# Kernel tuning notes

Hardware: AMD Instinct MI355X
Metric: run time of the kernel (lower is better)

Reference implementation:

```python
import jax, jax.numpy as jnp
import numpy as np

D_MODEL = 512
N_HEADS = 8
Q_SEQ_LEN = 1024
KV_SEQ_LEN = 1024
N_MODES = 64
D_HEAD = D_MODEL // N_HEADS

# FEDformer frequency_modes (deterministic/lowest branch): lowest n_modes freqs
Q_MODES = np.arange(min(N_MODES, Q_SEQ_LEN // 2))
KV_MODES = np.arange(min(N_MODES, KV_SEQ_LEN // 2))


def setup_inputs() -> dict:
    key = jax.random.key(0)
    kq, kk, kv, kwr, kwi = jax.random.split(key, 5)
    B = 8
    scale = 1.0 / (D_MODEL * D_MODEL)
    return {
        "query": jax.random.normal(kq, (B, N_HEADS, Q_SEQ_LEN, D_HEAD), jnp.float32),
        "key": jax.random.normal(kk, (B, N_HEADS, KV_SEQ_LEN, D_HEAD), jnp.float32),
        "value": jax.random.normal(kv, (B, N_HEADS, KV_SEQ_LEN, D_HEAD), jnp.float32),
        "weights_re": scale * jax.random.uniform(kwr, (N_HEADS, D_HEAD, D_HEAD, len(Q_MODES)), jnp.float32),
        "weights_im": scale * jax.random.uniform(kwi, (N_HEADS, D_HEAD, D_HEAD, len(Q_MODES)), jnp.float32),
    }


def reference(query, key, value, weights_re, weights_im):
    # value is accepted but unused by the original forward (FEA-f variant).
    B, H, L, D = query.shape
    q_modes = jnp.asarray(Q_MODES)
    kv_modes = jnp.asarray(KV_MODES)

    # [B,H,D,L] -> rfft along time -> gather selected frequency modes
    q_fft = jnp.fft.rfft(jnp.swapaxes(query, -2, -1), axis=-1)   # [B,H,D,L//2+1]
    k_fft = jnp.fft.rfft(jnp.swapaxes(key, -2, -1), axis=-1)     # [B,H,D,Lk//2+1]
    q_fft = jnp.take(q_fft, q_modes, axis=-1)                    # [B,H,D,Mq]
    k_fft = jnp.take(k_fft, kv_modes, axis=-1)                   # [B,H,D,Mk]

    # complex attention in frequency domain (no conjugation, as in torch einsum)
    scores_fft = jnp.einsum('bhdq,bhdk->bhqk', q_fft, k_fft)
    attn_fft = jnp.tanh(scores_fft)
    context_fft = jnp.einsum('bhqk,bhdk->bhdq', attn_fft, k_fft)  # [B,H,D,Mq]

    w = (weights_re + 1j * weights_im).astype(jnp.complex64)      # [H,D,D,Mq]
    context_fft = jnp.einsum('bhiq,hijq->bhjq', context_fft, w)   # [B,H,D,Mq]

    # scatter modes back into full rfft spectrum, then irfft
    out_fft = jnp.zeros((B, H, D, L // 2 + 1), jnp.complex64)
    out_fft = out_fft.at[..., q_modes].set(context_fft)
    d_model = H * D
    context = jnp.fft.irfft(out_fft / d_model / d_model, n=L, axis=-1)  # [B,H,D,L]
    return context
```

## Files before the change

### kernel.cpp

```cpp
#include <hip/hip_runtime.h>
#include <hip/hip_bf16.h>
#include <cmath>

#define BATCH 8
#define NH 8
#define BH 64
#define SEQ 1024
#define DH 64
#define NM 64

#define P_PLANE 4096
#define C2_OFF  4194304

__global__ __launch_bounds__(256) void k_dft(const float* __restrict__ q,
                                             const float* __restrict__ k,
                                             float* __restrict__ P) {
  const int bid = blockIdx.x;
  const int bh = bid & 63;
  const int inp = (bid >> 6) & 1;
  const int th = bid >> 7;
  const float* x = (inp ? k : q) + (size_t)bh * (SEQ * DH);

  __shared__ float xs[64][64];
  const int tid = threadIdx.x;
  const int dg = tid & 7;
  const int mg = tid >> 3;
  const int d0 = dg * 8;

  float accr[2][8] = {{0.f}}, acci[2][8] = {{0.f}};

  float stepc[2], steps_[2];
#pragma unroll
  for (int mi = 0; mi < 2; ++mi) {
    float ph = (float)(mg * 2 + mi) * (1.0f / 512.0f);
    stepc[mi] = cospif(ph);
    steps_[mi] = -sinpif(ph);
  }

  for (int ch = 0; ch < 8; ++ch) {
    const int t0g = th * 512 + ch * 64;
    const float4* src = reinterpret_cast<const float4*>(x + (size_t)t0g * DH);
    float4* dst = reinterpret_cast<float4*>(&xs[0][0]);
#pragma unroll
    for (int i = 0; i < 4; ++i) dst[tid + i * 256] = src[tid + i * 256];
    __syncthreads();

    float wr[2], wi[2];
#pragma unroll
    for (int mi = 0; mi < 2; ++mi) {
      int m = mg * 2 + mi;
      int p0 = (m * t0g) & 1023;
      float ph = (float)p0 * (1.0f / 512.0f);
      wr[mi] = cospif(ph);
      wi[mi] = -sinpif(ph);
    }

#pragma unroll 4
    for (int t = 0; t < 64; ++t) {
      float4 a = *reinterpret_cast<const float4*>(&xs[t][d0]);
      float4 b = *reinterpret_cast<const float4*>(&xs[t][d0 + 4]);
      float xv[8] = {a.x, a.y, a.z, a.w, b.x, b.y, b.z, b.w};
#pragma unroll
      for (int mi = 0; mi < 2; ++mi) {
        float cwr = wr[mi], cwi = wi[mi];
#pragma unroll
        for (int di = 0; di < 8; ++di) {
          accr[mi][di] = fmaf(cwr, xv[di], accr[mi][di]);
          acci[mi][di] = fmaf(cwi, xv[di], acci[mi][di]);
        }
        float nr = cwr * stepc[mi] - cwi * steps_[mi];
        float ni = cwr * steps_[mi] + cwi * stepc[mi];
        wr[mi] = nr; wi[mi] = ni;
      }
    }
    __syncthreads();
  }

  const size_t base = ((((size_t)inp * 2 + th) * 64 + bh) * 2) * P_PLANE;
#pragma unroll
  for (int mi = 0; mi < 2; ++mi) {
    int m = mg * 2 + mi;
    float* pr = P + base + (size_t)m * 64 + d0;
    float* pi = P + base + P_PLANE + (size_t)m * 64 + d0;
    *reinterpret_cast<float4*>(pr)     = make_float4(accr[mi][0], accr[mi][1], accr[mi][2], accr[mi][3]);
    *reinterpret_cast<float4*>(pr + 4) = make_float4(accr[mi][4], accr[mi][5], accr[mi][6], accr[mi][7]);
    *reinterpret_cast<float4*>(pi)     = make_float4(acci[mi][0], acci[mi][1], acci[mi][2], acci[mi][3]);
    *reinterpret_cast<float4*>(pi + 4) = make_float4(acci[mi][4], acci[mi][5], acci[mi][6], acci[mi][7]);
  }
}

__device__ __forceinline__ void ctanh_f(float x, float y, float& rr, float& ri) {
  float a = 2.0f * x, b = 2.0f * y;
  if (fabsf(a) > 20.0f) {
    rr = (a > 0.0f) ? 1.0f : -1.0f;
    ri = 0.0f;
  } else {
    float ea = expf(a), ena = expf(-a);
    float sb, cb;
    sincosf(b, &sb, &cb);
    float den = 0.5f * (ea + ena) + cb;
    rr = 0.5f * (ea - ena) / den;
    ri = sb / den;
  }
}

__global__ __launch_bounds__(256) void k_mid(const float* __restrict__ P,
                                             const float* __restrict__ wre,
                                             const float* __restrict__ wim,
                                             float* __restrict__ C2) {
  __shared__ float Kr[64][67], Ki[64][67];
  __shared__ float Qr[16][67], Qi[16][67];
  __shared__ float Ar[16][67], Ai[16][67];
  __shared__ float C1r[64][17], C1i[64][17];

  const int tid = threadIdx.x;
  const int bh = blockIdx.x >> 2;
  const int qq = blockIdx.x & 3;
  const int h = bh & 7;

  const size_t pq0 = (((size_t)0 * 2 + 0) * 64 + bh) * 2 * P_PLANE;
  const size_t pq1 = (((size_t)0 * 2 + 1) * 64 + bh) * 2 * P_PLANE;
  const size_t pk0 = (((size_t)1 * 2 + 0) * 64 + bh) * 2 * P_PLANE;
  const size_t pk1 = (((size_t)1 * 2 + 1) * 64 + bh) * 2 * P_PLANE;

  for (int idx = tid; idx < 4096; idx += 256) {
    int kk = idx >> 6, dd = idx & 63;
    Kr[kk][dd] = P[pk0 + idx] + P[pk1 + idx];
    Ki[kk][dd] = P[pk0 + P_PLANE + idx] + P[pk1 + P_PLANE + idx];
  }
  for (int idx = tid; idx < 1024; idx += 256) {
    int qi2 = idx >> 6, dd = idx & 63;
    int m = qq * 16 + qi2;
    Qr[qi2][dd] = P[pq0 + m * 64 + dd] + P[pq1 + m * 64 + dd];
    Qi[qi2][dd] = P[pq0 + P_PLANE + m * 64 + dd] + P[pq1 + P_PLANE + m * 64 + dd];
  }
  __syncthreads();

  {
    const int q = tid >> 4, k0 = (tid & 15) * 4;
    float sr[4] = {0.f}, si[4] = {0.f};
    for (int d = 0; d < 64; ++d) {
      float qr = Qr[q][d], qi = Qi[q][d];
#pragma unroll
      for (int j = 0; j < 4; ++j) {
        float kr = Kr[k0 + j][d], ki = Ki[k0 + j][d];
        sr[j] = fmaf(qr, kr, sr[j]); sr[j] = fmaf(-qi, ki, sr[j]);
        si[j] = fmaf(qr, ki, si[j]); si[j] = fmaf(qi, kr, si[j]);
      }
    }
#pragma unroll
    for (int j = 0; j < 4; ++j) {
      float rr, ri;
      ctanh_f(sr[j], si[j], rr, ri);
      Ar[q][k0 + j] = rr;
      Ai[q][k0 + j] = ri;
    }
  }
  __syncthreads();

  {
    const int q = tid >> 4, d0 = (tid & 15) * 4;
    float cr[4] = {0.f}, ci[4] = {0.f};
    for (int kk = 0; kk < 64; ++kk) {
      float ar = Ar[q][kk], ai = Ai[q][kk];
#pragma unroll
      for (int j = 0; j < 4; ++j) {
        float kr = Kr[kk][d0 + j], ki = Ki[kk][d0 + j];
        cr[j] = fmaf(ar, kr, cr[j]); cr[j] = fmaf(-ai, ki, cr[j]);
        ci[j] = fmaf(ar, ki, ci[j]); ci[j] = fmaf(ai, kr, ci[j]);
      }
    }
#pragma unroll
    for (int j = 0; j < 4; ++j) { C1r[d0 + j][q] = cr[j]; C1i[d0 + j][q] = ci[j]; }
  }
  __syncthreads();

  {
    const int ql = tid & 15, j0 = (tid >> 4) * 4;
    const int qg = qq * 16 + ql;
    float ar[4] = {0.f}, ai[4] = {0.f};
    for (int i = 0; i < 64; ++i) {
      float c1r = C1r[i][ql], c1i = C1i[i][ql];
      const size_t wb = (((size_t)h * 64 + i) * 64 + j0) * 64 + qg;
#pragma unroll
      for (int j = 0; j < 4; ++j) {
        float wr = wre[wb + (size_t)j * 64];
        float wi = wim[wb + (size_t)j * 64];
        ar[j] = fmaf(c1r, wr, ar[j]); ar[j] = fmaf(-c1i, wi, ar[j]);
        ai[j] = fmaf(c1r, wi, ai[j]); ai[j] = fmaf(c1i, wr, ai[j]);
      }
    }
#pragma unroll
    for (int j = 0; j < 4; ++j) {
      size_t o = (((size_t)bh * 64 + qg) * 64 + (j0 + j)) * 2;
      C2[o] = ar[j];
      C2[o + 1] = ai[j];
    }
  }
}

__global__ __launch_bounds__(256) void k_idft(const float* __restrict__ C2,
                                              float* __restrict__ out) {
  __shared__ float Cr[64][68], Ci[64][68];
  const int tid = threadIdx.x;
  const int bh = blockIdx.x >> 3;
  const int tc = blockIdx.x & 7;
  const float s = 1.0f / (512.0f * 512.0f * 1024.0f);

  for (int idx = tid; idx < 4096; idx += 256) {
    int m = idx >> 6, j = idx & 63;
    float f = (m == 0) ? s : 2.0f * s;
    Cr[m][j] = f * C2[((size_t)bh * 4096 + idx) * 2];
    Ci[m][j] = f * C2[((size_t)bh * 4096 + idx) * 2 + 1];
  }
  __syncthreads();

  const int tt = tid & 31, jg = tid >> 5;
  const int t0 = tc * 128 + tt * 4, j0 = jg * 8;

  float wc[4], wsn[4], sc[4], ss[4];
#pragma unroll
  for (int kk = 0; kk < 4; ++kk) {
    float ph = (float)((t0 + kk) & 1023) * (1.0f / 512.0f);
    sc[kk] = cospif(ph);
    ss[kk] = sinpif(ph);
    wc[kk] = 1.0f;
    wsn[kk] = 0.0f;
  }

  float acc[4][8] = {{0.f}};
  for (int m = 0; m < 64; ++m) {
    float4 c0 = *reinterpret_cast<const float4*>(&Cr[m][j0]);
    float4 c1 = *reinterpret_cast<const float4*>(&Cr[m][j0 + 4]);
    float4 e0 = *reinterpret_cast<const float4*>(&Ci[m][j0]);
    float4 e1 = *reinterpret_cast<const float4*>(&Ci[m][j0 + 4]);
    float crv[8] = {c0.x, c0.y, c0.z, c0.w, c1.x, c1.y, c1.z, c1.w};
    float civ[8] = {e0.x, e0.y, e0.z, e0.w, e1.x, e1.y, e1.z, e1.w};
#pragma unroll
    for (int kk = 0; kk < 4; ++kk) {
      float cw = wc[kk], sw = wsn[kk];
#pragma unroll
      for (int jj = 0; jj < 8; ++jj) {
        acc[kk][jj] = fmaf(crv[jj], cw, acc[kk][jj]);
        acc[kk][jj] = fmaf(-civ[jj], sw, acc[kk][jj]);
      }
      float nr = cw * sc[kk] - sw * ss[kk];
      float ni = cw * ss[kk] + sw * sc[kk];
      wc[kk] = nr; wsn[kk] = ni;
    }
  }

#pragma unroll
  for (int jj = 0; jj < 8; ++jj) {
    float4 v = make_float4(acc[0][jj], acc[1][jj], acc[2][jj], acc[3][jj]);
    *reinterpret_cast<float4*>(&out[(size_t)bh * 65536 + (size_t)(j0 + jj) * 1024 + t0]) = v;
  }
}

extern "C" void kernel_launch(void* const* d_in, const int* in_sizes, int n_in,
                              void* d_out, int out_size, void* d_ws, size_t ws_size,
                              hipStream_t stream) {
  const float* q   = (const float*)d_in[0];
  const float* k   = (const float*)d_in[1];
  const float* wre = (const float*)d_in[3];
  const float* wim = (const float*)d_in[4];
  float* out = (float*)d_out;
  float* ws  = (float*)d_ws;

  float* P  = ws;
  float* C2 = ws + C2_OFF;

  k_dft <<<256, 256, 0, stream>>>(q, k, P);
  k_mid <<<256, 256, 0, stream>>>(P, wre, wim, C2);
  k_idft<<<512, 256, 0, stream>>>(C2, out);
}
```

Baseline: 190.9 us.

## Split mode-mixing into separate kernel and double grid sizes for DFT and iDFT

After: 178.1 us. 1.07x faster.

```diff
diff --git a/kernel.cpp b/kernel.cpp
--- a/kernel.cpp
+++ b/kernel.cpp
@@ -10,7 +10,10 @@
 #define NM 64
 
 #define P_PLANE 4096
-#define C2_OFF  4194304
+#define P_FLOATS (2*4*64*2*4096)
+#define C1R_OFF  P_FLOATS
+#define C1I_OFF  (C1R_OFF + 64*64*64)
+#define C2_OFF   (C1I_OFF + 64*64*64)
 
 __global__ __launch_bounds__(256) void k_dft(const float* __restrict__ q,
                                              const float* __restrict__ k,
@@ -18,74 +21,62 @@
   const int bid = blockIdx.x;
   const int bh = bid & 63;
   const int inp = (bid >> 6) & 1;
-  const int th = bid >> 7;
+  const int tq = bid >> 7;
   const float* x = (inp ? k : q) + (size_t)bh * (SEQ * DH);
 
   __shared__ float xs[64][64];
   const int tid = threadIdx.x;
-  const int dg = tid & 7;
-  const int mg = tid >> 3;
-  const int d0 = dg * 8;
-
-  float accr[2][8] = {{0.f}}, acci[2][8] = {{0.f}};
-
-  float stepc[2], steps_[2];
-#pragma unroll
-  for (int mi = 0; mi < 2; ++mi) {
-    float ph = (float)(mg * 2 + mi) * (1.0f / 512.0f);
-    stepc[mi] = cospif(ph);
-    steps_[mi] = -sinpif(ph);
-  }
-
-  for (int ch = 0; ch < 8; ++ch) {
-    const int t0g = th * 512 + ch * 64;
+  const int m = tid >> 2;
+  const int d0 = (tid & 3) * 16;
+
+  float accr[16] = {0.f}, acci[16] = {0.f};
+
+  const float phs = (float)m * (1.0f / 512.0f);
+  const float stepc = cospif(phs);
+  const float steps = -sinpif(phs);
+
+  for (int ch = 0; ch < 4; ++ch) {
+    const int t0g = tq * 256 + ch * 64;
     const float4* src = reinterpret_cast<const float4*>(x + (size_t)t0g * DH);
     float4* dst = reinterpret_cast<float4*>(&xs[0][0]);
 #pragma unroll
     for (int i = 0; i < 4; ++i) dst[tid + i * 256] = src[tid + i * 256];
     __syncthreads();
 
-    float wr[2], wi[2];
-#pragma unroll
-    for (int mi = 0; mi < 2; ++mi) {
-      int m = mg * 2 + mi;
-      int p0 = (m * t0g) & 1023;
-      float ph = (float)p0 * (1.0f / 512.0f);
-      wr[mi] = cospif(ph);
-      wi[mi] = -sinpif(ph);
-    }
+    const int p0 = (m * t0g) & 1023;
+    const float ph0 = (float)p0 * (1.0f / 512.0f);
+    float wr = cospif(ph0);
+    float wi = -sinpif(ph0);
 
 #pragma unroll 4
     for (int t = 0; t < 64; ++t) {
       float4 a = *reinterpret_cast<const float4*>(&xs[t][d0]);
       float4 b = *reinterpret_cast<const float4*>(&xs[t][d0 + 4]);
-      float xv[8] = {a.x, a.y, a.z, a.w, b.x, b.y, b.z, b.w};
-#pragma unroll
-      for (int mi = 0; mi < 2; ++mi) {
-        float cwr = wr[mi], cwi = wi[mi];
-#pragma unroll
-        for (int di = 0; di < 8; ++di) {
-          accr[mi][di] = fmaf(cwr, xv[di], accr[mi][di]);
-          acci[mi][di] = fmaf(cwi, xv[di], acci[mi][di]);
-        }
-        float nr = cwr * stepc[mi] - cwi * steps_[mi];
-        float ni = cwr * steps_[mi] + cwi * stepc[mi];
-        wr[mi] = nr; wi[mi] = ni;
-      }
+      float4 c = *reinterpret_cast<const float4*>(&xs[t][d0 + 8]);
+      float4 e = *reinterpret_cast<const float4*>(&xs[t][d0 + 12]);
+      float xv[16] = {a.x, a.y, a.z, a.w, b.x, b.y, b.z, b.w,
+                      c.x, c.y, c.z, c.w, e.x, e.y, e.z, e.w};
+#pragma unroll
+      for (int di = 0; di < 16; ++di) {
+        accr[di] = fmaf(wr, xv[di], accr[di]);
+        acci[di] = fmaf(wi, xv[di], acci[di]);
+      }
+      float nr = wr * stepc - wi * steps;
+      float ni = wr * steps + wi * stepc;
+      wr = nr; wi = ni;
     }
     __syncthreads();
   }
 
-  const size_t base = ((((size_t)inp * 2 + th) * 64 + bh) * 2) * P_PLANE;
-#pragma unroll
-  for (int mi = 0; mi < 2; ++mi) {
-    int m = mg * 2 + mi;
-    float* pr = P + base + (size_t)m * 64 + d0;
-    float* pi = P + base + P_PLANE + (size_t)m * 64 + d0;
-    *reinterpret_cast<float4*>(pr)     = make_float4(accr[mi][0], accr[mi][1], accr[mi][2], accr[mi][3]);
-    *reinterpret_cast<float4*>(pr + 4) = make_float4(accr[mi][4], accr[mi][5], accr[mi][6], accr[mi][7]);
-    *reinterpret_cast<float4*>(pi)     = make_float4(acci[mi][0], acci[mi][1], acci[mi][2], acci[mi][3]);
-    *reinterpret_cast<float4*>(pi + 4) = make_float4(acci[mi][4], acci[mi][5], acci[mi][6], acci[mi][7]);
+  const size_t base = ((((size_t)inp * 4 + tq) * 64 + bh) * 2) * P_PLANE;
+  float* pr = P + base + (size_t)m * 64 + d0;
+  float* pi = P + base + P_PLANE + (size_t)m * 64 + d0;
+#pragma unroll
+  for (int i = 0; i < 4; ++i) {
+    *reinterpret_cast<float4*>(pr + i * 4) =
+        make_float4(accr[i * 4], accr[i * 4 + 1], accr[i * 4 + 2], accr[i * 4 + 3]);
+    *reinterpret_cast<float4*>(pi + i * 4) =
+        make_float4(acci[i * 4], acci[i * 4 + 1], acci[i * 4 + 2], acci[i * 4 + 3]);
   }
 }
 
@@ -104,35 +95,45 @@
   }
 }
 
-__global__ __launch_bounds__(256) void k_mid(const float* __restrict__ P,
-                                             const float* __restrict__ wre,
-                                             const float* __restrict__ wim,
-                                             float* __restrict__ C2) {
+__global__ __launch_bounds__(256) void k_mid_a(const float* __restrict__ P,
+                                               float* __restrict__ C1r,
+                                               float* __restrict__ C1i) {
   __shared__ float Kr[64][67], Ki[64][67];
   __shared__ float Qr[16][67], Qi[16][67];
   __shared__ float Ar[16][67], Ai[16][67];
-  __shared__ float C1r[64][17], C1i[64][17];
+  __shared__ float C1rs[64][17], C1is[64][17];
 
   const int tid = threadIdx.x;
   const int bh = blockIdx.x >> 2;
   const int qq = blockIdx.x & 3;
-  const int h = bh & 7;
-
-  const size_t pq0 = (((size_t)0 * 2 + 0) * 64 + bh) * 2 * P_PLANE;
-  const size_t pq1 = (((size_t)0 * 2 + 1) * 64 + bh) * 2 * P_PLANE;
-  const size_t pk0 = (((size_t)1 * 2 + 0) * 64 + bh) * 2 * P_PLANE;
-  const size_t pk1 = (((size_t)1 * 2 + 1) * 64 + bh) * 2 * P_PLANE;
+
+  size_t pq[4], pk[4];
+#pragma unroll
+  for (int t = 0; t < 4; ++t) {
+    pq[t] = (((size_t)(0 * 4 + t) * 64 + bh) * 2) * P_PLANE;
+    pk[t] = (((size_t)(1 * 4 + t) * 64 + bh) * 2) * P_PLANE;
+  }
 
   for (int idx = tid; idx < 4096; idx += 256) {
     int kk = idx >> 6, dd = idx & 63;
-    Kr[kk][dd] = P[pk0 + idx] + P[pk1 + idx];
-    Ki[kk][dd] = P[pk0 + P_PLANE + idx] + P[pk1 + P_PLANE + idx];
+    float r = 0.f, im = 0.f;
+#pragma unroll
+    for (int t = 0; t < 4; ++t) {
+      r += P[pk[t] + idx];
+      im += P[pk[t] + P_PLANE + idx];
+    }
+    Kr[kk][dd] = r; Ki[kk][dd] = im;
   }
   for (int idx = tid; idx < 1024; idx += 256) {
     int qi2 = idx >> 6, dd = idx & 63;
-    int m = qq * 16 + qi2;
-    Qr[qi2][dd] = P[pq0 + m * 64 + dd] + P[pq1 + m * 64 + dd];
-    Qi[qi2][dd] = P[pq0 + P_PLANE + m * 64 + dd] + P[pq1 + P_PLANE + m * 64 + dd];
+    int mm = qq * 16 + qi2;
+    float r = 0.f, im = 0.f;
+#pragma unroll
+    for (int t = 0; t < 4; ++t) {
+      r += P[pq[t] + mm * 64 + dd];
+      im += P[pq[t] + P_PLANE + mm * 64 + dd];
+    }
+    Qr[qi2][dd] = r; Qi[qi2][dd] = im;
   }
   __syncthreads();
 
@@ -171,31 +172,47 @@
       }
     }
 #pragma unroll
-    for (int j = 0; j < 4; ++j) { C1r[d0 + j][q] = cr[j]; C1i[d0 + j][q] = ci[j]; }
-  }
-  __syncthreads();
-
-  {
-    const int ql = tid & 15, j0 = (tid >> 4) * 4;
-    const int qg = qq * 16 + ql;
-    float ar[4] = {0.f}, ai[4] = {0.f};
-    for (int i = 0; i < 64; ++i) {
-      float c1r = C1r[i][ql], c1i = C1i[i][ql];
-      const size_t wb = (((size_t)h * 64 + i) * 64 + j0) * 64 + qg;
-#pragma unroll
-      for (int j = 0; j < 4; ++j) {
-        float wr = wre[wb + (size_t)j * 64];
-        float wi = wim[wb + (size_t)j * 64];
-        ar[j] = fmaf(c1r, wr, ar[j]); ar[j] = fmaf(-c1i, wi, ar[j]);
-        ai[j] = fmaf(c1r, wi, ai[j]); ai[j] = fmaf(c1i, wr, ai[j]);
-      }
-    }
-#pragma unroll
-    for (int j = 0; j < 4; ++j) {
-      size_t o = (((size_t)bh * 64 + qg) * 64 + (j0 + j)) * 2;
-      C2[o] = ar[j];
-      C2[o + 1] = ai[j];
-    }
+    for (int j = 0; j < 4; ++j) { C1rs[d0 + j][q] = cr[j]; C1is[d0 + j][q] = ci[j]; }
+  }
+  __syncthreads();
+
+  for (int idx = tid; idx < 1024; idx += 256) {
+    int i = idx >> 4, ql = idx & 15;
+    size_t o = ((size_t)bh * 64 + i) * 64 + qq * 16 + ql;
+    C1r[o] = C1rs[i][ql];
+    C1i[o] = C1is[i][ql];
+  }
+}
+
+__global__ __launch_bounds__(64) void k_mid_b(const float* __restrict__ C1r,
+                                              const float* __restrict__ C1i,
+                                              const float* __restrict__ wre,
+                                              const float* __restrict__ wim,
+                                              float* __restrict__ C2) {
+  const int bid = blockIdx.x;
+  const int j = bid & 63;
+  const int h = (bid >> 6) & 7;
+  const int bq = bid >> 9;
+  const int lane = threadIdx.x;
+
+  float ar[2] = {0.f, 0.f}, ai[2] = {0.f, 0.f};
+  for (int i = 0; i < 64; ++i) {
+    size_t wo = (((size_t)h * 64 + i) * 64 + j) * 64 + lane;
+    float wr = wre[wo], wi = wim[wo];
+#pragma unroll
+    for (int bb = 0; bb < 2; ++bb) {
+      int bh = (bq * 2 + bb) * 8 + h;
+      size_t co = ((size_t)bh * 64 + i) * 64 + lane;
+      float c1r = C1r[co], c1i = C1i[co];
+      ar[bb] = fmaf(c1r, wr, ar[bb]); ar[bb] = fmaf(-c1i, wi, ar[bb]);
+      ai[bb] = fmaf(c1r, wi, ai[bb]); ai[bb] = fmaf(c1i, wr, ai[bb]);
+    }
+  }
+#pragma unroll
+  for (int bb = 0; bb < 2; ++bb) {
+    int bh = (bq * 2 + bb) * 8 + h;
+    *reinterpret_cast<float2*>(&C2[(((size_t)bh * 64 + j) * 64 + lane) * 2]) =
+        make_float2(ar[bb], ai[bb]);
   }
 }
 
@@ -203,24 +220,25 @@
                                               float* __restrict__ out) {
   __shared__ float Cr[64][68], Ci[64][68];
   const int tid = threadIdx.x;
-  const int bh = blockIdx.x >> 3;
-  const int tc = blockIdx.x & 7;
+  const int bh = blockIdx.x >> 4;
+  const int tc = blockIdx.x & 15;
   const float s = 1.0f / (512.0f * 512.0f * 1024.0f);
 
   for (int idx = tid; idx < 4096; idx += 256) {
-    int m = idx >> 6, j = idx & 63;
+    int j = idx >> 6, m = idx & 63;
     float f = (m == 0) ? s : 2.0f * s;
-    Cr[m][j] = f * C2[((size_t)bh * 4096 + idx) * 2];
-    Ci[m][j] = f * C2[((size_t)bh * 4096 + idx) * 2 + 1];
-  }
-  __syncthreads();
-
-  const int tt = tid & 31, jg = tid >> 5;
-  const int t0 = tc * 128 + tt * 4, j0 = jg * 8;
-
-  float wc[4], wsn[4], sc[4], ss[4];
-#pragma unroll
-  for (int kk = 0; kk < 4; ++kk) {
+    float2 c = *reinterpret_cast<const float2*>(&C2[(((size_t)bh * 64 + j) * 64 + m) * 2]);
+    Cr[m][j] = f * c.x;
+    Ci[m][j] = f * c.y;
+  }
+  __syncthreads();
+
+  const int tg = tid & 31, jg = tid >> 5;
+  const int t0 = tc * 64 + tg * 2, j0 = jg * 8;
+
+  float sc[2], ss[2], wc[2], wsn[2];
+#pragma unroll
+  for (int kk = 0; kk < 2; ++kk) {
     float ph = (float)((t0 + kk) & 1023) * (1.0f / 512.0f);
     sc[kk] = cospif(ph);
     ss[kk] = sinpif(ph);
@@ -228,7 +246,7 @@
     wsn[kk] = 0.0f;
   }
 
-  float acc[4][8] = {{0.f}};
+  float acc[2][8] = {{0.f}};
   for (int m = 0; m < 64; ++m) {
     float4 c0 = *reinterpret_cast<const float4*>(&Cr[m][j0]);
     float4 c1 = *reinterpret_cast<const float4*>(&Cr[m][j0 + 4]);
@@ -237,7 +255,7 @@
     float crv[8] = {c0.x, c0.y, c0.z, c0.w, c1.x, c1.y, c1.z, c1.w};
     float civ[8] = {e0.x, e0.y, e0.z, e0.w, e1.x, e1.y, e1.z, e1.w};
 #pragma unroll
-    for (int kk = 0; kk < 4; ++kk) {
+    for (int kk = 0; kk < 2; ++kk) {
       float cw = wc[kk], sw = wsn[kk];
 #pragma unroll
       for (int jj = 0; jj < 8; ++jj) {
@@ -252,8 +270,8 @@
 
 #pragma unroll
   for (int jj = 0; jj < 8; ++jj) {
-    float4 v = make_float4(acc[0][jj], acc[1][jj], acc[2][jj], acc[3][jj]);
-    *reinterpret_cast<float4*>(&out[(size_t)bh * 65536 + (size_t)(j0 + jj) * 1024 + t0]) = v;
+    *reinterpret_cast<float2*>(&out[(size_t)bh * 65536 + (size_t)(j0 + jj) * 1024 + t0]) =
+        make_float2(acc[0][jj], acc[1][jj]);
   }
 }
 
@@ -267,10 +285,13 @@
   float* out = (float*)d_out;
   float* ws  = (float*)d_ws;
 
-  float* P  = ws;
-  float* C2 = ws + C2_OFF;
-
-  k_dft <<<256, 256, 0, stream>>>(q, k, P);
-  k_mid <<<256, 256, 0, stream>>>(P, wre, wim, C2);
-  k_idft<<<512, 256, 0, stream>>>(C2, out);
-}
+  float* P   = ws;
+  float* C1r = ws + C1R_OFF;
+  float* C1i = ws + C1I_OFF;
+  float* C2  = ws + C2_OFF;
+
+  k_dft  <<<512,  256, 0, stream>>>(q, k, P);
+  k_mid_a<<<256,  256, 0, stream>>>(P, C1r, C1i);
+  k_mid_b<<<2048,  64, 0, stream>>>(C1r, C1i, wre, wim, C2);
+  k_idft <<<1024, 256, 0, stream>>>(C2, out);
+}
```
